# Performance work log

Measured on AMD Instinct MI355X. Metric: run time of the kernel, lower is better.

The kernel has to match this reference:

```python
import math
import jax, jax.numpy as jnp
import numpy as np

KS, UP, DOWN = 4, 2, 1
P1 = (KS - 1) // 2          # 1
P2 = KS - 1 - P1            # 2


def make_kernel(ks: int) -> jnp.ndarray:
    k = np.array([math.comb(ks - 1, i) for i in range(ks)], dtype=np.float32)
    k = k / k.sum()
    return jnp.asarray(np.outer(k, k))  # [ky, kx], separable binomial


def setup_inputs() -> dict:
    key = jax.random.key(0)
    imgs = jax.random.normal(key, (16, 128, 128, 128), dtype=jnp.float32)
    return {"imgs": imgs, "kernel": make_kernel(KS)}


def reference(imgs, kernel):
    # upfirdn2d: zero-insert upsample by UP, pad (P1,P2) each spatial side,
    # depthwise cross-correlate with `kernel`, downsample by DOWN.
    # lhs_dilation implements the zero-insert upsample without materializing it;
    # XLA applies padding after lhs dilation, matching pad-after-upsample.
    n, c, h, w = imgs.shape
    rhs = jnp.broadcast_to(kernel[None, None], (c, 1, kernel.shape[0], kernel.shape[1]))
    out = jax.lax.conv_general_dilated(
        imgs, rhs,
        window_strides=(DOWN, DOWN),
        padding=[(P1, P2), (P1, P2)],
        lhs_dilation=(UP, UP),
        dimension_numbers=("NCHW", "OIHW", "NCHW"),
        feature_group_count=c,
    )
    return out  # [N, C, H*UP, W*UP]
```

## Files before the change

kernel.cpp:

```cpp
#include <hip/hip_runtime.h>


#define IH 128
#define IW 128

__global__ __launch_bounds__(256) void blur_up2_kernel(
    const float* __restrict__ in, const float* __restrict__ ker,
    float* __restrict__ out, int oh, int ow) {
    int id = blockIdx.x * 256 + threadIdx.x;
    int ix = id & (IW - 1);
    int iy = (id >> 7) & (IH - 1);
    int nc = id >> 14;

    const float* ib = in + (size_t)nc * (IH * IW) + (size_t)iy * IW + ix;
    bool xin = (ix < IW - 1);
    bool yin = (iy < IH - 1);

    float a = ib[0];
    float b = xin ? ib[1] : 0.f;
    float c = yin ? ib[IW] : 0.f;
    float d = (xin && yin) ? ib[IW + 1] : 0.f;

    float K00 = ker[0],  K01 = ker[1],  K02 = ker[2],  K03 = ker[3];
    float K10 = ker[4],  K11 = ker[5],  K12 = ker[6],  K13 = ker[7];
    float K20 = ker[8],  K21 = ker[9],  K22 = ker[10], K23 = ker[11];
    float K30 = ker[12], K31 = ker[13], K32 = ker[14], K33 = ker[15];

    float o00 = K11 * a + K13 * b + K31 * c + K33 * d;
    float o01 = K10 * a + K12 * b + K30 * c + K32 * d;
    float o10 = K01 * a + K03 * b + K21 * c + K23 * d;
    float o11 = K00 * a + K02 * b + K20 * c + K22 * d;

    int ox = 2 * ix, oy = 2 * iy;
    size_t ob = (size_t)nc * ((size_t)oh * ow) + (size_t)oy * ow + ox;
    bool xs = (ox + 1 < ow);
    bool ys = (oy + 1 < oh);

    out[ob] = o00;
    if (xs) out[ob + 1] = o01;
    if (ys) out[ob + ow] = o10;
    if (xs && ys) out[ob + ow + 1] = o11;
}

extern "C" void kernel_launch(void* const* d_in, const int* in_sizes, int n_in,
                              void* d_out, int out_size, void* d_ws, size_t ws_size,
                              hipStream_t stream) {
    const float* imgs = (const float*)d_in[0];
    const float* ker  = (const float*)d_in[1];
    float* out        = (float*)d_out;

    const int NC = 16 * 128;
    int ohw = out_size / NC;
    int ow = (ohw == 256 * 256) ? 256 : 255;
    int oh = ow;

    int total = NC * IH * IW;
    int blocks = total / 256;
    blur_up2_kernel<<<blocks, 256, 0, stream>>>(imgs, ker, out, oh, ow);
}
```

Before: 657.7 us.

## Restructure upsample blur as row-pair gather with LDS staging and XCD-aware block swizzle

Each block now handles one input row pair and produces two full output rows. The two input rows are staged in shared memory and each thread writes one output column, so global stores are contiguous per row rather than strided pairs. Block IDs are remapped across the 8 XCDs so neighbouring rows land on the same die for L2 reuse. In exchange it adds a syncthreads and extra index math, and each input row is read by two blocks.

Result: slower. 750.4 us (+14.1%).

```diff
diff --git a/kernel.cpp b/kernel.cpp
--- a/kernel.cpp
+++ b/kernel.cpp
@@ -4,42 +4,57 @@
 #define IH 128
 #define IW 128
 
-__global__ __launch_bounds__(256) void blur_up2_kernel(
+__global__ __launch_bounds__(256) void blur_up2_gather(
     const float* __restrict__ in, const float* __restrict__ ker,
     float* __restrict__ out, int oh, int ow) {
-    int id = blockIdx.x * 256 + threadIdx.x;
-    int ix = id & (IW - 1);
-    int iy = (id >> 7) & (IH - 1);
-    int nc = id >> 14;
+    int nwg = gridDim.x;
+    int cpx = nwg >> 3;
+    int bid = blockIdx.x;
+    int lb  = (bid & 7) * cpx + (bid >> 3);
 
-    const float* ib = in + (size_t)nc * (IH * IW) + (size_t)iy * IW + ix;
-    bool xin = (ix < IW - 1);
-    bool yin = (iy < IH - 1);
+    int p  = lb & 127;
+    int nc = lb >> 7;
 
-    float a = ib[0];
-    float b = xin ? ib[1] : 0.f;
-    float c = yin ? ib[IW] : 0.f;
-    float d = (xin && yin) ? ib[IW + 1] : 0.f;
+    __shared__ float r0[IW + 4];
+    __shared__ float r1[IW + 4];
+
+    int t = threadIdx.x;
+    const float* ib = in + (size_t)nc * (IH * IW);
+    if (t < IW) {
+        r0[t] = ib[(size_t)p * IW + t];
+    } else {
+        int tt = t - IW;
+        r1[tt] = (p + 1 < IH) ? ib[(size_t)(p + 1) * IW + tt] : 0.f;
+    }
+    if (t == 0) { r0[IW] = 0.f; r1[IW] = 0.f; }
 
     float K00 = ker[0],  K01 = ker[1],  K02 = ker[2],  K03 = ker[3];
     float K10 = ker[4],  K11 = ker[5],  K12 = ker[6],  K13 = ker[7];
     float K20 = ker[8],  K21 = ker[9],  K22 = ker[10], K23 = ker[11];
     float K30 = ker[12], K31 = ker[13], K32 = ker[14], K33 = ker[15];
 
-    float o00 = K11 * a + K13 * b + K31 * c + K33 * d;
-    float o01 = K10 * a + K12 * b + K30 * c + K32 * d;
-    float o10 = K01 * a + K03 * b + K21 * c + K23 * d;
-    float o11 = K00 * a + K02 * b + K20 * c + K22 * d;
+    __syncthreads();
 
-    int ox = 2 * ix, oy = 2 * iy;
+    int ox = t;
+    if (ox >= ow) return;
+    int  q  = ox >> 1;
+    bool hx = (ox & 1) != 0;
+
+    float a0 = r0[q], a1 = r0[q + 1];
+    float b0 = r1[q], b1 = r1[q + 1];
+
+    float w1a = hx ? K10 : K11, w1b = hx ? K12 : K13;
+    float w3a = hx ? K30 : K31, w3b = hx ? K32 : K33;
+    float w0a = hx ? K00 : K01, w0b = hx ? K02 : K03;
+    float w2a = hx ? K20 : K21, w2b = hx ? K22 : K23;
+
+    float o0 = w1a * a0 + w1b * a1 + w3a * b0 + w3b * b1;
+    float o1 = w0a * a0 + w0b * a1 + w2a * b0 + w2b * b1;
+
+    int oy = 2 * p;
     size_t ob = (size_t)nc * ((size_t)oh * ow) + (size_t)oy * ow + ox;
-    bool xs = (ox + 1 < ow);
-    bool ys = (oy + 1 < oh);
-
-    out[ob] = o00;
-    if (xs) out[ob + 1] = o01;
-    if (ys) out[ob + ow] = o10;
-    if (xs && ys) out[ob + ow + 1] = o11;
+    out[ob] = o0;
+    if (oy + 1 < oh) out[ob + ow] = o1;
 }
 
 extern "C" void kernel_launch(void* const* d_in, const int* in_sizes, int n_in,
@@ -54,7 +69,6 @@
     int ow = (ohw == 256 * 256) ? 256 : 255;
     int oh = ow;
 
-    int total = NC * IH * IW;
-    int blocks = total / 256;
-    blur_up2_kernel<<<blocks, 256, 0, stream>>>(imgs, ker, out, oh, ow);
+    int blocks = NC * ((oh + 1) / 2);
+    blur_up2_gather<<<blocks, 256, 0, stream>>>(imgs, ker, out, oh, ow);
 }
```

## Process two input columns per thread with vectorized float4 stores and block swizzle

Applied to the files above, without the earlier changes.

Each thread now handles two adjacent input pixels, loading them as float2 pairs and writing four output columns per row with float4 stores instead of scalar stores. This halves the thread count and cuts per-element memory instructions on a write-heavy, bandwidth-bound upsample. Block indices are also remapped with a stride-8 swizzle, likely to spread work across XCDs or memory channels. Stores use 4-byte-aligned float4s to cover the odd-width case, which may split into unaligned accesses when ow is 255.

Measured after the change: 640.4 us. 1.03x faster.

```diff
diff --git a/kernel.cpp b/kernel.cpp
--- a/kernel.cpp
+++ b/kernel.cpp
@@ -4,42 +4,67 @@
 #define IH 128
 #define IW 128
 
-__global__ __launch_bounds__(256) void blur_up2_kernel(
+typedef float f2 __attribute__((ext_vector_type(2)));
+typedef float f4 __attribute__((ext_vector_type(4)));
+typedef f4 uf4 __attribute__((aligned(4)));
+
+__global__ __launch_bounds__(256) void blur_up2_vec(
     const float* __restrict__ in, const float* __restrict__ ker,
     float* __restrict__ out, int oh, int ow) {
-    int id = blockIdx.x * 256 + threadIdx.x;
-    int ix = id & (IW - 1);
-    int iy = (id >> 7) & (IH - 1);
-    int nc = id >> 14;
+    int bid = blockIdx.x;
+    int lb  = (bid & 7) * (int)(gridDim.x >> 3) + (bid >> 3);
+    int id  = lb * 256 + (int)threadIdx.x;
 
-    const float* ib = in + (size_t)nc * (IH * IW) + (size_t)iy * IW + ix;
-    bool xin = (ix < IW - 1);
-    bool yin = (iy < IH - 1);
+    int j  = id & 63;
+    int iy = (id >> 6) & 127;
+    int nc = id >> 13;
 
-    float a = ib[0];
-    float b = xin ? ib[1] : 0.f;
-    float c = yin ? ib[IW] : 0.f;
-    float d = (xin && yin) ? ib[IW + 1] : 0.f;
+    const float* ib = in + ((size_t)nc << 14) + ((size_t)iy << 7) + (j << 1);
+
+    f2 r0 = *reinterpret_cast<const f2*>(ib);
+    float a = r0.x, b = r0.y;
+    float e = (j < 63) ? ib[2] : 0.f;
+
+    float c = 0.f, d = 0.f, f = 0.f;
+    if (iy < IH - 1) {
+        f2 r1 = *reinterpret_cast<const f2*>(ib + IW);
+        c = r1.x; d = r1.y;
+        f = (j < 63) ? ib[IW + 2] : 0.f;
+    }
 
     float K00 = ker[0],  K01 = ker[1],  K02 = ker[2],  K03 = ker[3];
     float K10 = ker[4],  K11 = ker[5],  K12 = ker[6],  K13 = ker[7];
     float K20 = ker[8],  K21 = ker[9],  K22 = ker[10], K23 = ker[11];
     float K30 = ker[12], K31 = ker[13], K32 = ker[14], K33 = ker[15];
 
-    float o00 = K11 * a + K13 * b + K31 * c + K33 * d;
-    float o01 = K10 * a + K12 * b + K30 * c + K32 * d;
-    float o10 = K01 * a + K03 * b + K21 * c + K23 * d;
-    float o11 = K00 * a + K02 * b + K20 * c + K22 * d;
+    f4 o0, o1;
+    o0.x = K11 * a + K13 * b + K31 * c + K33 * d;
+    o0.y = K10 * a + K12 * b + K30 * c + K32 * d;
+    o0.z = K11 * b + K13 * e + K31 * d + K33 * f;
+    o0.w = K10 * b + K12 * e + K30 * d + K32 * f;
+    o1.x = K01 * a + K03 * b + K21 * c + K23 * d;
+    o1.y = K00 * a + K02 * b + K20 * c + K22 * d;
+    o1.z = K01 * b + K03 * e + K21 * d + K23 * f;
+    o1.w = K00 * b + K02 * e + K20 * d + K22 * f;
 
-    int ox = 2 * ix, oy = 2 * iy;
+    int oy = iy << 1, ox = j << 2;
     size_t ob = (size_t)nc * ((size_t)oh * ow) + (size_t)oy * ow + ox;
-    bool xs = (ox + 1 < ow);
-    bool ys = (oy + 1 < oh);
+    bool odd = (oy + 1 < oh);
 
-    out[ob] = o00;
-    if (xs) out[ob + 1] = o01;
-    if (ys) out[ob + ow] = o10;
-    if (xs && ys) out[ob + ow + 1] = o11;
+    if (ox + 3 < ow) {
+        *reinterpret_cast<uf4*>(out + ob) = o0;
+        if (odd) *reinterpret_cast<uf4*>(out + ob + ow) = o1;
+    } else {
+        int rem = ow - ox;
+        if (rem > 0) out[ob] = o0.x;
+        if (rem > 1) out[ob + 1] = o0.y;
+        if (rem > 2) out[ob + 2] = o0.z;
+        if (odd) {
+            if (rem > 0) out[ob + ow] = o1.x;
+            if (rem > 1) out[ob + ow + 1] = o1.y;
+            if (rem > 2) out[ob + ow + 2] = o1.z;
+        }
+    }
 }
 
 extern "C" void kernel_launch(void* const* d_in, const int* in_sizes, int n_in,
@@ -54,7 +79,7 @@
     int ow = (ohw == 256 * 256) ? 256 : 255;
     int oh = ow;
 
-    int total = NC * IH * IW;
+    int total  = NC * IH * (IW / 2);
     int blocks = total / 256;
-    blur_up2_kernel<<<blocks, 256, 0, stream>>>(imgs, ker, out, oh, ow);
+    blur_up2_vec<<<blocks, 256, 0, stream>>>(imgs, ker, out, oh, ow);
 }
```
